# Kernel optimization log

Measured on AMD Instinct MI355X. Metric: run time of the kernel, lower is better.

The kernel has to match this reference:

```python
import jax, jax.numpy as jnp
import numpy as np

N = 8192          # n_nodes
E = 262144        # n_edges (avg degree 32)
F_IN, H1, H2, H3, OUT6 = 512, 256, 128, 64, 6


def setup_inputs() -> dict:
    key = jax.random.key(0)
    ks = jax.random.split(key, 12)
    x = jax.random.normal(ks[0], (N, F_IN), dtype=jnp.float32)
    adj_rows = jax.random.randint(ks[1], (E,), 0, N, dtype=jnp.int32)
    adj_cols = jax.random.randint(ks[2], (E,), 0, N, dtype=jnp.int32)
    adj_vals = jax.random.uniform(ks[3], (E,), dtype=jnp.float32)
    s = 0.05  # small init scale
    W1 = jax.random.normal(ks[4], (F_IN, H1), dtype=jnp.float32) * s
    W2 = jax.random.normal(ks[5], (H1, H2), dtype=jnp.float32) * s
    W3 = jax.random.normal(ks[6], (H1, H2), dtype=jnp.float32) * s
    dense_W = jax.random.normal(ks[7], (H2, H3), dtype=jnp.float32) * s
    dense_b = jax.random.normal(ks[8], (H3,), dtype=jnp.float32) * s
    dense1_W = jax.random.normal(ks[9], (H3, OUT6), dtype=jnp.float32) * s
    dense1_b = jax.random.normal(ks[10], (OUT6,), dtype=jnp.float32) * s
    return {"x": x, "adj_rows": adj_rows, "adj_cols": adj_cols, "adj_vals": adj_vals,
            "W1": W1, "W2": W2, "W3": W3,
            "dense_W": dense_W, "dense_b": dense_b,
            "dense1_W": dense1_W, "dense1_b": dense1_b}


def reference(x, adj_rows, adj_cols, adj_vals, W1, W2, W3,
              dense_W, dense_b, dense1_W, dense1_b):
    n = x.shape[0]

    def spmm(support):  # sparse [N,N] @ dense [N,D] via COO gather/segment-sum
        gathered = adj_vals[:, None] * support[adj_cols]  # [E, D]
        return jax.ops.segment_sum(gathered, adj_rows, num_segments=n)

    # eval mode: dropout = identity
    hidden1 = jax.nn.relu(spmm(x @ W1))          # gc1, act=relu
    mu0 = spmm(hidden1 @ W2)                     # gc2, act=identity
    logvar0 = spmm(hidden1 @ W3)                 # gc3, act=identity
    # LinearNet.forward never applies its activation -> plain affine
    mu = mu0 @ dense_W + dense_b                 # [N, H3]
    logvar = logvar0 @ dense_W + dense_b         # [N, H3]
    z = mu                                       # reparameterize in eval mode
    adj_rec = z @ z.T                            # InnerProductDecoder, act=identity
    out6 = z @ dense1_W + dense1_b               # dense1, [N, 6]
    return (adj_rec, out6, mu, logvar)
```

## Files before the change

kernel.cpp:

```cpp
#include <hip/hip_runtime.h>
#include <hip/hip_bf16.h>

#define N_NODES 8192
#define N_EDGES 262144

typedef __attribute__((ext_vector_type(8))) short short8;
typedef __attribute__((ext_vector_type(4))) float f32x4;

__device__ __forceinline__ unsigned short f2bf(float f) {
    unsigned int u = __float_as_uint(f);
    u = (u + 0x7fffu + ((u >> 16) & 1u)) >> 16;
    return (unsigned short)u;
}
__device__ __forceinline__ float bf2f(unsigned short h) {
    return __uint_as_float((unsigned int)h << 16);
}

__global__ void k_hist(const int* __restrict__ rows, int* __restrict__ counts) {
    int e = blockIdx.x * 256 + threadIdx.x;
    if (e < N_EDGES) atomicAdd(&counts[rows[e]], 1);
}

__global__ void k_scan(const int* __restrict__ counts, int* __restrict__ offs) {
    __shared__ int part[1024];
    int t = threadIdx.x;
    int base = t * 8;
    int loc[8];
    int s = 0;
#pragma unroll
    for (int i = 0; i < 8; i++) { loc[i] = s; s += counts[base + i]; }
    part[t] = s;
    __syncthreads();
    for (int off = 1; off < 1024; off <<= 1) {
        int v = (t >= off) ? part[t - off] : 0;
        __syncthreads();
        part[t] += v;
        __syncthreads();
    }
    int prev = (t == 0) ? 0 : part[t - 1];
#pragma unroll
    for (int i = 0; i < 8; i++) offs[base + i] = prev + loc[i];
    if (t == 1023) offs[N_NODES] = part[1023];
}

__global__ void k_scatter(const int* __restrict__ rows, const int* __restrict__ colsIn,
                          const float* __restrict__ valsIn, const int* __restrict__ offs,
                          int* __restrict__ cursor, int* __restrict__ colsOut,
                          float* __restrict__ valsOut) {
    int e = blockIdx.x * 256 + threadIdx.x;
    if (e >= N_EDGES) return;
    int r = rows[e];
    int p = atomicAdd(&cursor[r], 1);
    int idx = offs[r] + p;
    colsOut[idx] = colsIn[e];
    valsOut[idx] = valsIn[e];
}

__global__ void k_conv_x(const float* __restrict__ in, ushort* __restrict__ out) {
    int i = blockIdx.x * 256 + threadIdx.x;
    float4 v = ((const float4*)in)[i];
    ushort4 o = make_ushort4(f2bf(v.x), f2bf(v.y), f2bf(v.z), f2bf(v.w));
    ((ushort4*)out)[i] = o;
}

__global__ void k_w1t(const float* __restrict__ W, ushort* __restrict__ Wt) {
    int i = blockIdx.x * 256 + threadIdx.x;
    int k = i >> 8, n = i & 255;
    Wt[n * 512 + k] = f2bf(W[i]);
}

__global__ void k_w23t(const float* __restrict__ W2, const float* __restrict__ W3,
                       ushort* __restrict__ Wt) {
    int i = blockIdx.x * 256 + threadIdx.x;
    int n = i >> 8, k = i & 255;
    float v = (n < 128) ? W2[k * 128 + n] : W3[k * 128 + (n - 128)];
    Wt[i] = f2bf(v);
}

__global__ __launch_bounds__(256) void k_gemm_mfma(const ushort* __restrict__ A,
                                                   const ushort* __restrict__ Bt,
                                                   ushort* __restrict__ C,
                                                   int K, int ldc) {
    int t = threadIdx.x;
    int lane = t & 63;
    int w = t >> 6;
    int I = blockIdx.y * 128 + (w >> 1) * 64;
    int J = blockIdx.x * 128 + (w & 1) * 64;
    int r = lane & 15;
    int koff = (lane >> 4) * 8;
    const ushort* Ab = A + (size_t)(I + r) * K + koff;
    const ushort* Bb = Bt + (size_t)(J + r) * K + koff;
    size_t rs = (size_t)16 * K;

    short8 a0[4], b0[4], a1[4], b1[4];
#pragma unroll
    for (int m = 0; m < 4; m++) {
        a0[m] = *(const short8*)(Ab + m * rs);
        b0[m] = *(const short8*)(Bb + m * rs);
    }
    f32x4 acc[4][4];
#pragma unroll
    for (int m = 0; m < 4; m++)
#pragma unroll
        for (int n = 0; n < 4; n++) acc[m][n] = (f32x4){0.f, 0.f, 0.f, 0.f};

    int nk = K >> 5;
    for (int kt = 0; kt < nk; kt += 2) {
        int o1 = (kt + 1) << 5;
#pragma unroll
        for (int m = 0; m < 4; m++) {
            a1[m] = *(const short8*)(Ab + m * rs + o1);
            b1[m] = *(const short8*)(Bb + m * rs + o1);
        }
#pragma unroll
        for (int m = 0; m < 4; m++)
#pragma unroll
            for (int n = 0; n < 4; n++)
                acc[m][n] = __builtin_amdgcn_mfma_f32_16x16x32_bf16(a0[m], b0[n], acc[m][n], 0, 0, 0);
        if (kt + 2 < nk) {
            int o2 = (kt + 2) << 5;
#pragma unroll
            for (int m = 0; m < 4; m++) {
                a0[m] = *(const short8*)(Ab + m * rs + o2);
                b0[m] = *(const short8*)(Bb + m * rs + o2);
            }
        }
#pragma unroll
        for (int m = 0; m < 4; m++)
#pragma unroll
            for (int n = 0; n < 4; n++)
                acc[m][n] = __builtin_amdgcn_mfma_f32_16x16x32_bf16(a1[m], b1[n], acc[m][n], 0, 0, 0);
    }

    int crow = (lane >> 4) * 4;
    int ccol = lane & 15;
#pragma unroll
    for (int m = 0; m < 4; m++)
#pragma unroll
        for (int rg = 0; rg < 4; rg++) {
            size_t row = (size_t)(I + m * 16 + crow + rg);
#pragma unroll
            for (int n = 0; n < 4; n++)
                C[row * ldc + J + n * 16 + ccol] = f2bf(acc[m][n][rg]);
        }
}

__global__ __launch_bounds__(256) void k_spmm_h(const int* __restrict__ offs,
                                                const int* __restrict__ cols,
                                                const float* __restrict__ vals,
                                                const ushort* __restrict__ in,
                                                ushort* __restrict__ outh,
                                                float* __restrict__ outf, int relu) {
    const int row = blockIdx.x;
    const int d = threadIdx.x;
    int s = offs[row], e = offs[row + 1];
    float acc = 0.f;
    __shared__ int sc[256];
    __shared__ float sv[256];
    for (int base = s; base < e; base += 256) {
        int n = e - base;
        if (n > 256) n = 256;
        if (d < n) { sc[d] = cols[base + d]; sv[d] = vals[base + d]; }
        __syncthreads();
        for (int i = 0; i < n; i++)
            acc += sv[i] * bf2f(in[(size_t)sc[i] * 256 + d]);
        __syncthreads();
    }
    if (relu) acc = fmaxf(acc, 0.f);
    if (outh) outh[(size_t)row * 256 + d] = f2bf(acc);
    else outf[(size_t)row * 256 + d] = acc;
}

__global__ __launch_bounds__(256) void k_dense(const float* __restrict__ A,
                                               const float* __restrict__ B,
                                               const float* __restrict__ bias,
                                               float* __restrict__ mu,
                                               float* __restrict__ logvar,
                                               ushort* __restrict__ Zh) {
    __shared__ float sA[16][68];
    __shared__ float sB[16][68];
    int tx = threadIdx.x, ty = threadIdx.y;
    int t = ty * 16 + tx;
    int row0 = blockIdx.x * 64;
    int am = t >> 2, ak = (t & 3) * 4;
    int bk = t >> 4, bn = (t & 15) * 4;
    float acc[4][4] = {};
    for (int k0 = 0; k0 < 128; k0 += 16) {
        float4 av = *(const float4*)&A[(size_t)(row0 + am) * 128 + k0 + ak];
        float4 bv = *(const float4*)&B[(size_t)(k0 + bk) * 64 + bn];
        sA[ak + 0][am] = av.x; sA[ak + 1][am] = av.y;
        sA[ak + 2][am] = av.z; sA[ak + 3][am] = av.w;
        *(float4*)&sB[bk][bn] = bv;
        __syncthreads();
#pragma unroll
        for (int k = 0; k < 16; k++) {
            float4 a4 = *(const float4*)&sA[k][ty * 4];
            float4 b4 = *(const float4*)&sB[k][tx * 4];
            float ar[4] = {a4.x, a4.y, a4.z, a4.w};
            float br[4] = {b4.x, b4.y, b4.z, b4.w};
#pragma unroll
            for (int a = 0; a < 4; a++)
#pragma unroll
                for (int b = 0; b < 4; b++) acc[a][b] += ar[a] * br[b];
        }
        __syncthreads();
    }
#pragma unroll
    for (int a = 0; a < 4; a++) {
        int vrow = row0 + ty * 4 + a;
        int col = tx * 4;
        float4 rv = make_float4(acc[a][0] + bias[col], acc[a][1] + bias[col + 1],
                                acc[a][2] + bias[col + 2], acc[a][3] + bias[col + 3]);
        int nr = vrow >> 1;
        if (vrow & 1) {
            *(float4*)&logvar[(size_t)nr * 64 + col] = rv;
        } else {
            *(float4*)&mu[(size_t)nr * 64 + col] = rv;
            ushort4 h = make_ushort4(f2bf(rv.x), f2bf(rv.y), f2bf(rv.z), f2bf(rv.w));
            *(ushort4*)&Zh[(size_t)nr * 64 + col] = h;
        }
    }
}

__global__ __launch_bounds__(256) void k_out6(const float* __restrict__ Z,
                                              const float* __restrict__ W,
                                              const float* __restrict__ b,
                                              float* __restrict__ out) {
    __shared__ float sW[384];
    int t = threadIdx.x;
    for (int i = t; i < 384; i += 256) sW[i] = W[i];
    __syncthreads();
    int row = blockIdx.x * 256 + t;
    float acc[6];
#pragma unroll
    for (int j = 0; j < 6; j++) acc[j] = b[j];
    for (int k = 0; k < 64; k++) {
        float zv = Z[(size_t)row * 64 + k];
#pragma unroll
        for (int j = 0; j < 6; j++) acc[j] += zv * sW[k * 6 + j];
    }
#pragma unroll
    for (int j = 0; j < 6; j++) out[(size_t)row * 6 + j] = acc[j];
}

__global__ __launch_bounds__(256) void k_zzt_mfma(const ushort* __restrict__ Zh,
                                                  float* __restrict__ C) {
    int t = threadIdx.x;
    int lane = t & 63;
    int w = t >> 6;
    int I = blockIdx.y * 128 + (w >> 1) * 64;
    int J = blockIdx.x * 128 + (w & 1) * 64;
    int r = lane & 15;
    int koff = (lane >> 4) * 8;

    short8 a[4][2], b[4][2];
#pragma unroll
    for (int m = 0; m < 4; m++) {
#pragma unroll
        for (int kk = 0; kk < 2; kk++) {
            a[m][kk] = *(const short8*)(Zh + (size_t)(I + m * 16 + r) * 64 + kk * 32 + koff);
            b[m][kk] = *(const short8*)(Zh + (size_t)(J + m * 16 + r) * 64 + kk * 32 + koff);
        }
    }
    f32x4 acc[4][4];
#pragma unroll
    for (int m = 0; m < 4; m++)
#pragma unroll
        for (int n = 0; n < 4; n++) acc[m][n] = (f32x4){0.f, 0.f, 0.f, 0.f};

#pragma unroll
    for (int kk = 0; kk < 2; kk++)
#pragma unroll
        for (int m = 0; m < 4; m++)
#pragma unroll
            for (int n = 0; n < 4; n++)
                acc[m][n] = __builtin_amdgcn_mfma_f32_16x16x32_bf16(a[m][kk], b[n][kk],
                                                                    acc[m][n], 0, 0, 0);

    int crow = (lane >> 4) * 4;
    int ccol = lane & 15;
#pragma unroll
    for (int m = 0; m < 4; m++)
#pragma unroll
        for (int rg = 0; rg < 4; rg++) {
            size_t row = (size_t)(I + m * 16 + crow + rg);
#pragma unroll
            for (int n = 0; n < 4; n++)
                C[row * 8192 + J + n * 16 + ccol] = acc[m][n][rg];
        }
}

extern "C" void kernel_launch(void* const* d_in, const int* in_sizes, int n_in,
                              void* d_out, int out_size, void* d_ws, size_t ws_size,
                              hipStream_t stream) {
    const float* x        = (const float*)d_in[0];
    const int*   adj_rows = (const int*)d_in[1];
    const int*   adj_cols = (const int*)d_in[2];
    const float* adj_vals = (const float*)d_in[3];
    const float* W1       = (const float*)d_in[4];
    const float* W2       = (const float*)d_in[5];
    const float* W3       = (const float*)d_in[6];
    const float* dense_W  = (const float*)d_in[7];
    const float* dense_b  = (const float*)d_in[8];
    const float* dense1_W = (const float*)d_in[9];
    const float* dense1_b = (const float*)d_in[10];

    char* p = (char*)d_ws;
    int* counts  = (int*)p;    p += 8192 * 4;
    int* cursor  = (int*)p;    p += 8192 * 4;
    int* offs    = (int*)p;    p += 8224 * 4;
    int* scol    = (int*)p;    p += (size_t)N_EDGES * 4;
    float* sval  = (float*)p;  p += (size_t)N_EDGES * 4;
    ushort* xh   = (ushort*)p; p += (size_t)8192 * 512 * 2;
    ushort* W1t  = (ushort*)p; p += (size_t)256 * 512 * 2;
    ushort* W23t = (ushort*)p; p += (size_t)256 * 256 * 2;
    ushort* XW1h = (ushort*)p; p += (size_t)8192 * 256 * 2;
    ushort* Hidh = (ushort*)p; p += (size_t)8192 * 256 * 2;
    ushort* Tbh  = (ushort*)p; p += (size_t)8192 * 256 * 2;
    float* Mb    = (float*)p;  p += (size_t)8192 * 256 * 4;
    ushort* Zh   = (ushort*)p; p += (size_t)8192 * 64 * 2;

    float* out     = (float*)d_out;
    float* adj_rec = out;
    float* out6    = out + (size_t)8192 * 8192;
    float* mu      = out6 + (size_t)8192 * 6;
    float* logvar  = mu + (size_t)8192 * 64;

    hipMemsetAsync(counts, 0, 2 * 8192 * 4, stream);
    k_hist<<<N_EDGES / 256, 256, 0, stream>>>(adj_rows, counts);
    k_scan<<<1, 1024, 0, stream>>>(counts, offs);
    k_scatter<<<N_EDGES / 256, 256, 0, stream>>>(adj_rows, adj_cols, adj_vals, offs, cursor,
                                                 scol, sval);
    k_conv_x<<<4096, 256, 0, stream>>>(x, xh);
    k_w1t<<<512, 256, 0, stream>>>(W1, W1t);
    k_w23t<<<256, 256, 0, stream>>>(W2, W3, W23t);

    k_gemm_mfma<<<dim3(2, 64), 256, 0, stream>>>(xh, W1t, XW1h, 512, 256);
    k_spmm_h<<<8192, 256, 0, stream>>>(offs, scol, sval, XW1h, Hidh, nullptr, 1);
    k_gemm_mfma<<<dim3(2, 64), 256, 0, stream>>>(Hidh, W23t, Tbh, 256, 256);
    k_spmm_h<<<8192, 256, 0, stream>>>(offs, scol, sval, Tbh, nullptr, Mb, 0);
    k_dense<<<256, dim3(16, 16), 0, stream>>>(Mb, dense_W, dense_b, mu, logvar, Zh);
    k_out6<<<32, 256, 0, stream>>>(mu, dense1_W, dense1_b, out6);
    k_zzt_mfma<<<dim3(64, 64), 256, 0, stream>>>(Zh, adj_rec);
}
```

Baseline: 425.5 us.

## Merge prep kernels, retile GEMM, warp-per-row SpMM, MFMA dense layer

Combines the histogram, x conversion and weight transposes into one multi-role prep kernel, which cuts the number of launches. The feature GEMM moves to 128-thread blocks with 64-column tiles, giving twice as many blocks. SpMM now handles one row per wavefront, with each lane loading four bf16 values and prefetching the next column and value, in place of one row per block with shared-memory staging. The second SpMM writes bf16 instead of fp32, and the dense layer becomes an MFMA bf16 kernel over a pre-transposed weight, which adds rounding error to mu and logvar.

```diff
diff --git a/kernel.cpp b/kernel.cpp
--- a/kernel.cpp
+++ b/kernel.cpp
@@ -14,11 +14,6 @@
 }
 __device__ __forceinline__ float bf2f(unsigned short h) {
     return __uint_as_float((unsigned int)h << 16);
-}
-
-__global__ void k_hist(const int* __restrict__ rows, int* __restrict__ counts) {
-    int e = blockIdx.x * 256 + threadIdx.x;
-    if (e < N_EDGES) atomicAdd(&counts[rows[e]], 1);
 }
 
 __global__ void k_scan(const int* __restrict__ counts, int* __restrict__ offs) {
@@ -56,36 +51,44 @@
     valsOut[idx] = valsIn[e];
 }
 
-__global__ void k_conv_x(const float* __restrict__ in, ushort* __restrict__ out) {
-    int i = blockIdx.x * 256 + threadIdx.x;
-    float4 v = ((const float4*)in)[i];
-    ushort4 o = make_ushort4(f2bf(v.x), f2bf(v.y), f2bf(v.z), f2bf(v.w));
-    ((ushort4*)out)[i] = o;
-}
-
-__global__ void k_w1t(const float* __restrict__ W, ushort* __restrict__ Wt) {
-    int i = blockIdx.x * 256 + threadIdx.x;
-    int k = i >> 8, n = i & 255;
-    Wt[n * 512 + k] = f2bf(W[i]);
-}
-
-__global__ void k_w23t(const float* __restrict__ W2, const float* __restrict__ W3,
-                       ushort* __restrict__ Wt) {
-    int i = blockIdx.x * 256 + threadIdx.x;
-    int n = i >> 8, k = i & 255;
-    float v = (n < 128) ? W2[k * 128 + n] : W3[k * 128 + (n - 128)];
-    Wt[i] = f2bf(v);
-}
-
-__global__ __launch_bounds__(256) void k_gemm_mfma(const ushort* __restrict__ A,
+__global__ void k_prep(const int* __restrict__ rows, int* __restrict__ counts,
+                       const float* __restrict__ x, ushort* __restrict__ xh,
+                       const float* __restrict__ W1, ushort* __restrict__ W1t,
+                       const float* __restrict__ W2, const float* __restrict__ W3,
+                       ushort* __restrict__ W23t,
+                       const float* __restrict__ dW, ushort* __restrict__ Wdt) {
+    int b = blockIdx.x, t = threadIdx.x;
+    if (b < 1024) {
+        atomicAdd(&counts[rows[b * 256 + t]], 1);
+    } else if (b < 5120) {
+        int i = (b - 1024) * 256 + t;
+        float4 v = ((const float4*)x)[i];
+        ((ushort4*)xh)[i] = make_ushort4(f2bf(v.x), f2bf(v.y), f2bf(v.z), f2bf(v.w));
+    } else if (b < 5632) {
+        int i = (b - 5120) * 256 + t;
+        int k = i >> 8, n = i & 255;
+        W1t[n * 512 + k] = f2bf(W1[i]);
+    } else if (b < 5888) {
+        int i = (b - 5632) * 256 + t;
+        int n = i >> 8, k = i & 255;
+        float v = (n < 128) ? W2[k * 128 + n] : W3[k * 128 + (n - 128)];
+        W23t[i] = f2bf(v);
+    } else {
+        int i = (b - 5888) * 256 + t;
+        int j = i >> 7, k = i & 127;
+        Wdt[i] = f2bf(dW[k * 64 + j]);
+    }
+}
+
+__global__ __launch_bounds__(128) void k_gemm_mfma(const ushort* __restrict__ A,
                                                    const ushort* __restrict__ Bt,
                                                    ushort* __restrict__ C,
                                                    int K, int ldc) {
     int t = threadIdx.x;
     int lane = t & 63;
     int w = t >> 6;
-    int I = blockIdx.y * 128 + (w >> 1) * 64;
-    int J = blockIdx.x * 128 + (w & 1) * 64;
+    int I = blockIdx.y * 128 + w * 64;
+    int J = blockIdx.x * 64;
     int r = lane & 15;
     int koff = (lane >> 4) * 8;
     const ushort* Ab = A + (size_t)(I + r) * K + koff;
@@ -145,81 +148,94 @@
         }
 }
 
-__global__ __launch_bounds__(256) void k_spmm_h(const int* __restrict__ offs,
-                                                const int* __restrict__ cols,
-                                                const float* __restrict__ vals,
-                                                const ushort* __restrict__ in,
-                                                ushort* __restrict__ outh,
-                                                float* __restrict__ outf, int relu) {
-    const int row = blockIdx.x;
-    const int d = threadIdx.x;
-    int s = offs[row], e = offs[row + 1];
-    float acc = 0.f;
-    __shared__ int sc[256];
-    __shared__ float sv[256];
-    for (int base = s; base < e; base += 256) {
-        int n = e - base;
-        if (n > 256) n = 256;
-        if (d < n) { sc[d] = cols[base + d]; sv[d] = vals[base + d]; }
-        __syncthreads();
-        for (int i = 0; i < n; i++)
-            acc += sv[i] * bf2f(in[(size_t)sc[i] * 256 + d]);
-        __syncthreads();
-    }
-    if (relu) acc = fmaxf(acc, 0.f);
-    if (outh) outh[(size_t)row * 256 + d] = f2bf(acc);
-    else outf[(size_t)row * 256 + d] = acc;
-}
-
-__global__ __launch_bounds__(256) void k_dense(const float* __restrict__ A,
-                                               const float* __restrict__ B,
-                                               const float* __restrict__ bias,
-                                               float* __restrict__ mu,
-                                               float* __restrict__ logvar,
-                                               ushort* __restrict__ Zh) {
-    __shared__ float sA[16][68];
-    __shared__ float sB[16][68];
-    int tx = threadIdx.x, ty = threadIdx.y;
-    int t = ty * 16 + tx;
-    int row0 = blockIdx.x * 64;
-    int am = t >> 2, ak = (t & 3) * 4;
-    int bk = t >> 4, bn = (t & 15) * 4;
-    float acc[4][4] = {};
-    for (int k0 = 0; k0 < 128; k0 += 16) {
-        float4 av = *(const float4*)&A[(size_t)(row0 + am) * 128 + k0 + ak];
-        float4 bv = *(const float4*)&B[(size_t)(k0 + bk) * 64 + bn];
-        sA[ak + 0][am] = av.x; sA[ak + 1][am] = av.y;
-        sA[ak + 2][am] = av.z; sA[ak + 3][am] = av.w;
-        *(float4*)&sB[bk][bn] = bv;
-        __syncthreads();
-#pragma unroll
-        for (int k = 0; k < 16; k++) {
-            float4 a4 = *(const float4*)&sA[k][ty * 4];
-            float4 b4 = *(const float4*)&sB[k][tx * 4];
-            float ar[4] = {a4.x, a4.y, a4.z, a4.w};
-            float br[4] = {b4.x, b4.y, b4.z, b4.w};
-#pragma unroll
-            for (int a = 0; a < 4; a++)
-#pragma unroll
-                for (int b = 0; b < 4; b++) acc[a][b] += ar[a] * br[b];
-        }
-        __syncthreads();
-    }
-#pragma unroll
-    for (int a = 0; a < 4; a++) {
-        int vrow = row0 + ty * 4 + a;
-        int col = tx * 4;
-        float4 rv = make_float4(acc[a][0] + bias[col], acc[a][1] + bias[col + 1],
-                                acc[a][2] + bias[col + 2], acc[a][3] + bias[col + 3]);
-        int nr = vrow >> 1;
-        if (vrow & 1) {
-            *(float4*)&logvar[(size_t)nr * 64 + col] = rv;
-        } else {
-            *(float4*)&mu[(size_t)nr * 64 + col] = rv;
-            ushort4 h = make_ushort4(f2bf(rv.x), f2bf(rv.y), f2bf(rv.z), f2bf(rv.w));
-            *(ushort4*)&Zh[(size_t)nr * 64 + col] = h;
-        }
-    }
+__global__ __launch_bounds__(256) void k_spmm_v2(const int* __restrict__ offs,
+                                                 const int* __restrict__ cols,
+                                                 const float* __restrict__ vals,
+                                                 const ushort* __restrict__ in,
+                                                 ushort* __restrict__ out, int relu) {
+    int w = threadIdx.x >> 6;
+    int lane = threadIdx.x & 63;
+    int row = blockIdx.x * 4 + w;
+    int colo = lane * 4;
+    int i = offs[row], e = offs[row + 1];
+    float4 acc = make_float4(0.f, 0.f, 0.f, 0.f);
+    int c = 0;
+    float v = 0.f;
+    if (i < e) { c = cols[i]; v = vals[i]; }
+    while (i < e) {
+        int cn = 0;
+        float vn = 0.f;
+        if (i + 1 < e) { cn = cols[i + 1]; vn = vals[i + 1]; }
+        ushort4 u = *(const ushort4*)&in[(size_t)c * 256 + colo];
+        acc.x += v * bf2f(u.x);
+        acc.y += v * bf2f(u.y);
+        acc.z += v * bf2f(u.z);
+        acc.w += v * bf2f(u.w);
+        c = cn; v = vn; ++i;
+    }
+    if (relu) {
+        acc.x = fmaxf(acc.x, 0.f); acc.y = fmaxf(acc.y, 0.f);
+        acc.z = fmaxf(acc.z, 0.f); acc.w = fmaxf(acc.w, 0.f);
+    }
+    *(ushort4*)&out[(size_t)row * 256 + colo] =
+        make_ushort4(f2bf(acc.x), f2bf(acc.y), f2bf(acc.z), f2bf(acc.w));
+}
+
+__global__ __launch_bounds__(256) void k_dense_mfma(const ushort* __restrict__ A,
+                                                    const ushort* __restrict__ Wdt,
+                                                    const float* __restrict__ bias,
+                                                    float* __restrict__ mu,
+                                                    float* __restrict__ logvar,
+                                                    ushort* __restrict__ Zh) {
+    int t = threadIdx.x;
+    int lane = t & 63;
+    int w = t >> 6;
+    int I = blockIdx.x * 256 + w * 64;
+    int r = lane & 15;
+    int koff = (lane >> 4) * 8;
+
+    f32x4 acc[4][4];
+#pragma unroll
+    for (int m = 0; m < 4; m++)
+#pragma unroll
+        for (int n = 0; n < 4; n++) acc[m][n] = (f32x4){0.f, 0.f, 0.f, 0.f};
+
+#pragma unroll
+    for (int kk = 0; kk < 4; kk++) {
+        short8 a[4], b[4];
+#pragma unroll
+        for (int m = 0; m < 4; m++)
+            a[m] = *(const short8*)(A + (size_t)(I + m * 16 + r) * 128 + kk * 32 + koff);
+#pragma unroll
+        for (int n = 0; n < 4; n++)
+            b[n] = *(const short8*)(Wdt + (size_t)(n * 16 + r) * 128 + kk * 32 + koff);
+#pragma unroll
+        for (int m = 0; m < 4; m++)
+#pragma unroll
+            for (int n = 0; n < 4; n++)
+                acc[m][n] = __builtin_amdgcn_mfma_f32_16x16x32_bf16(a[m], b[n], acc[m][n], 0, 0, 0);
+    }
+
+    int crow = (lane >> 4) * 4;
+    int ccol = lane & 15;
+#pragma unroll
+    for (int m = 0; m < 4; m++)
+#pragma unroll
+        for (int rg = 0; rg < 4; rg++) {
+            int vrow = I + m * 16 + crow + rg;
+            int nr = vrow >> 1;
+#pragma unroll
+            for (int n = 0; n < 4; n++) {
+                int col = n * 16 + ccol;
+                float val = acc[m][n][rg] + bias[col];
+                if (vrow & 1) {
+                    logvar[(size_t)nr * 64 + col] = val;
+                } else {
+                    mu[(size_t)nr * 64 + col] = val;
+                    Zh[(size_t)nr * 64 + col] = f2bf(val);
+                }
+            }
+        }
 }
 
 __global__ __launch_bounds__(256) void k_out6(const float* __restrict__ Z,
@@ -314,10 +330,11 @@
     ushort* xh   = (ushort*)p; p += (size_t)8192 * 512 * 2;
     ushort* W1t  = (ushort*)p; p += (size_t)256 * 512 * 2;
     ushort* W23t = (ushort*)p; p += (size_t)256 * 256 * 2;
+    ushort* Wdt  = (ushort*)p; p += (size_t)64 * 128 * 2;
     ushort* XW1h = (ushort*)p; p += (size_t)8192 * 256 * 2;
     ushort* Hidh = (ushort*)p; p += (size_t)8192 * 256 * 2;
     ushort* Tbh  = (ushort*)p; p += (size_t)8192 * 256 * 2;
-    float* Mb    = (float*)p;  p += (size_t)8192 * 256 * 4;
+    ushort* Mbh  = (ushort*)p; p += (size_t)8192 * 256 * 2;
     ushort* Zh   = (ushort*)p; p += (size_t)8192 * 64 * 2;
 
     float* out     = (float*)d_out;
@@ -327,19 +344,17 @@
     float* logvar  = mu + (size_t)8192 * 64;
 
     hipMemsetAsync(counts, 0, 2 * 8192 * 4, stream);
-    k_hist<<<N_EDGES / 256, 256, 0, stream>>>(adj_rows, counts);
+    k_prep<<<5920, 256, 0, stream>>>(adj_rows, counts, x, xh, W1, W1t, W2, W3, W23t,
+                                     dense_W, Wdt);
     k_scan<<<1, 1024, 0, stream>>>(counts, offs);
     k_scatter<<<N_EDGES / 256, 256, 0, stream>>>(adj_rows, adj_cols, adj_vals, offs, cursor,
                                                  scol, sval);
-    k_conv_x<<<4096, 256, 0, stream>>>(x, xh);
-    k_w1t<<<512, 256, 0, stream>>>(W1, W1t);
-    k_w23t<<<256, 256, 0, stream>>>(W2, W3, W23t);
-
-    k_gemm_mfma<<<dim3(2, 64), 256, 0, stream>>>(xh, W1t, XW1h, 512, 256);
-    k_spmm_h<<<8192, 256, 0, stream>>>(offs, scol, sval, XW1h, Hidh, nullptr, 1);
-    k_gemm_mfma<<<dim3(2, 64), 256, 0, stream>>>(Hidh, W23t, Tbh, 256, 256);
-    k_spmm_h<<<8192, 256, 0, stream>>>(offs, scol, sval, Tbh, nullptr, Mb, 0);
-    k_dense<<<256, dim3(16, 16), 0, stream>>>(Mb, dense_W, dense_b, mu, logvar, Zh);
+
+    k_gemm_mfma<<<dim3(4, 64), 128, 0, stream>>>(xh, W1t, XW1h, 512, 256);
+    k_spmm_v2<<<2048, 256, 0, stream>>>(offs, scol, sval, XW1h, Hidh, 1);
+    k_gemm_mfma<<<dim3(4, 64), 128, 0, stream>>>(Hidh, W23t, Tbh, 256, 256);
+    k_spmm_v2<<<2048, 256, 0, stream>>>(offs, scol, sval, Tbh, Mbh, 0);
+    k_dense_mfma<<<64, 256, 0, stream>>>(Mbh, Wdt, dense_b, mu, logvar, Zh);
     k_out6<<<32, 256, 0, stream>>>(mu, dense1_W, dense1_b, out6);
     k_zzt_mfma<<<dim3(64, 64), 256, 0, stream>>>(Zh, adj_rec);
 }
```

New measurement: 418.8 us. About the same (-1.6%).
